# Kernel optimization log

Hardware: AMD Instinct MI355X
Metric: run time of the kernel (lower is better)

## Reference

```python
import jax, jax.numpy as jnp
import numpy as np

MAX_FRAMES = 4096  # static output capacity = T_phoneme * max_duration
PAD_VALUE = 0.0


def setup_inputs() -> dict:
    key = jax.random.key(0)
    k1, k2, k3, k4 = jax.random.split(key, 4)
    B, C, T = 16, 512, 512
    xs = jax.random.normal(k1, (B, C, T), dtype=jnp.float32)
    notepitch = jax.random.uniform(k2, (B, T), dtype=jnp.float32)
    ds = jax.random.randint(k3, (B, T), 0, 8, dtype=jnp.int32)
    x_lengths = jax.random.randint(k4, (B,), 0, 512, dtype=jnp.int32)
    return {"xs": xs, "notepitch": notepitch, "ds": ds, "x_lengths": x_lengths}


def _length_regulate(xs, notepitch, ds):
    # xs: (B, C, T), notepitch: (B, T), ds: (B, T) int durations
    # Replicate: ds[ds.sum(dim=1)==0] = 1 (fill all-zero duration rows with 1)
    row_zero = (ds.sum(axis=1) == 0)[:, None]  # (B, 1)
    ds = jnp.where(row_zero, jnp.ones_like(ds), ds)

    xs_t = jnp.transpose(xs, (0, 2, 1))  # (B, T, C)
    cum = jnp.cumsum(ds, axis=1)         # (B, T) exclusive-end offsets
    total = cum[:, -1]                   # (B,) frame lengths

    pos = jnp.arange(MAX_FRAMES, dtype=cum.dtype)  # (T_out,)
    # For each output frame position, which source token does it come from?
    # token j covers positions [cum[j-1], cum[j]) -> searchsorted(cum, pos, 'right')
    idx = jax.vmap(lambda c: jnp.searchsorted(c, pos, side="right"))(cum)  # (B, T_out)
    T = ds.shape[1]
    idx = jnp.clip(idx, 0, T - 1)
    mask = pos[None, :] < total[:, None]  # (B, T_out) valid frames

    # Gather expanded features: repeat_interleave as a gather
    out = jnp.take_along_axis(xs_t, idx[:, :, None], axis=1)  # (B, T_out, C)
    out = jnp.where(mask[:, :, None], out, jnp.asarray(PAD_VALUE, out.dtype))
    out = jnp.transpose(out, (0, 2, 1))  # (B, C, T_out)

    pitch = jnp.take_along_axis(notepitch, idx, axis=1)  # (B, T_out)
    pitch = jnp.where(mask, pitch, jnp.asarray(PAD_VALUE, pitch.dtype))
    return out, pitch, total


def reference(xs, notepitch, ds, x_lengths):
    # notepitch is detached in the original forward
    out, pitch, total = _length_regulate(xs, jax.lax.stop_gradient(notepitch), ds)
    return out, pitch, total.astype(jnp.int32)
```

## Files before the change

### kernel.cpp

```cpp
#include <hip/hip_runtime.h>

#define MAXF 4096

__global__ __launch_bounds__(512) void lr_prep(
    const float* __restrict__ notepitch,
    const int* __restrict__ ds,
    int* __restrict__ idx_ws,
    float* __restrict__ pitch_out,
    float* __restrict__ total_out,
    int T)
{
    const int b = blockIdx.x;
    const int t = threadIdx.x;

    __shared__ int cum[512];
    __shared__ int idx_sh[MAXF];

    int v = (t < T) ? ds[b * T + t] : 0;
    cum[t] = v;
    __syncthreads();

    for (int off = 1; off < 512; off <<= 1) {
        int x = cum[t];
        int y = (t >= off) ? cum[t - off] : 0;
        __syncthreads();
        cum[t] = x + y;
        __syncthreads();
    }

    int total = cum[T - 1];
    if (total == 0) {
        cum[t] = t + 1;
        total = T;
    }
    __syncthreads();

    for (int p = t; p < MAXF; p += 512) idx_sh[p] = -1;
    __syncthreads();

    if (t < T) {
        int lo = (t > 0) ? cum[t - 1] : 0;
        int hi = cum[t];
        for (int p = lo; p < hi; ++p) idx_sh[p] = t;
    }
    __syncthreads();

    for (int p = t; p < MAXF; p += 512) {
        int id = idx_sh[p];
        idx_ws[b * MAXF + p] = id;
        pitch_out[(size_t)b * MAXF + p] = (id >= 0) ? notepitch[b * T + id] : 0.0f;
    }
    if (t == 0) total_out[b] = (float)total;
}

__global__ __launch_bounds__(256) void lr_gather(
    const float* __restrict__ xs,
    const int* __restrict__ idx_ws,
    float* __restrict__ out,
    int T, int C)
{
    const int row = blockIdx.x;
    const int b = row / C;
    const float* __restrict__ xrow = xs + (size_t)row * T;
    const int* __restrict__ irow  = idx_ws + b * MAXF;
    float* __restrict__ orow      = out + (size_t)row * MAXF;

    const int t = threadIdx.x;
#pragma unroll
    for (int i = 0; i < MAXF / (256 * 4); ++i) {
        int p4 = (i * 256 + t) * 4;
        int4 id = *reinterpret_cast<const int4*>(irow + p4);
        float4 v;
        v.x = (id.x >= 0) ? xrow[id.x] : 0.0f;
        v.y = (id.y >= 0) ? xrow[id.y] : 0.0f;
        v.z = (id.z >= 0) ? xrow[id.z] : 0.0f;
        v.w = (id.w >= 0) ? xrow[id.w] : 0.0f;
        *reinterpret_cast<float4*>(orow + p4) = v;
    }
}

extern "C" void kernel_launch(void* const* d_in, const int* in_sizes, int n_in,
                              void* d_out, int out_size, void* d_ws, size_t ws_size,
                              hipStream_t stream) {
    const float* xs        = (const float*)d_in[0];
    const float* notepitch = (const float*)d_in[1];
    const int*   ds        = (const int*)d_in[2];

    const int B = in_sizes[3];
    const int T = in_sizes[1] / B;
    const int C = in_sizes[0] / (B * T);

    float* out       = (float*)d_out;
    float* pitch_out = out + (size_t)B * C * MAXF;
    float* total_out = pitch_out + (size_t)B * MAXF;

    int* idx_ws = (int*)d_ws;

    lr_prep<<<B, 512, 0, stream>>>(notepitch, ds, idx_ws, pitch_out, total_out, T);
    lr_gather<<<B * C, 256, 0, stream>>>(xs, idx_ws, out, T, C);
}
```

Baseline: 32.58 us.

## Fuse prefix-sum index build into gather kernel with channel grouping

Merges the prep and gather kernels into one. Each block recomputes the per-batch cumulative durations and frame index map in shared memory, then gathers 8 channels, so the global index workspace and the second launch go away. The scan is repeated C/8 times per batch, which adds redundant shared-memory work and barriers to every block. A clamp on the fill range to MAXF is also added.

```diff
diff --git a/kernel.cpp b/kernel.cpp
--- a/kernel.cpp
+++ b/kernel.cpp
@@ -1,17 +1,20 @@
 #include <hip/hip_runtime.h>
 
 #define MAXF 4096
+#define CG 8
 
-__global__ __launch_bounds__(512) void lr_prep(
+__global__ __launch_bounds__(512) void lr_fused(
+    const float* __restrict__ xs,
     const float* __restrict__ notepitch,
     const int* __restrict__ ds,
-    int* __restrict__ idx_ws,
+    float* __restrict__ out,
     float* __restrict__ pitch_out,
     float* __restrict__ total_out,
-    int T)
+    int T, int C)
 {
-    const int b = blockIdx.x;
-    const int t = threadIdx.x;
+    const int b  = blockIdx.y;
+    const int cg = blockIdx.x;
+    const int t  = threadIdx.x;
 
     __shared__ int cum[512];
     __shared__ int idx_sh[MAXF];
@@ -41,41 +44,36 @@
     if (t < T) {
         int lo = (t > 0) ? cum[t - 1] : 0;
         int hi = cum[t];
+        if (hi > MAXF) hi = MAXF;
         for (int p = lo; p < hi; ++p) idx_sh[p] = t;
     }
     __syncthreads();
 
-    for (int p = t; p < MAXF; p += 512) {
-        int id = idx_sh[p];
-        idx_ws[b * MAXF + p] = id;
-        pitch_out[(size_t)b * MAXF + p] = (id >= 0) ? notepitch[b * T + id] : 0.0f;
+    const float* __restrict__ xbase = xs  + ((size_t)b * C + (size_t)cg * CG) * T;
+    float* __restrict__       obase = out + ((size_t)b * C + (size_t)cg * CG) * MAXF;
+
+#pragma unroll
+    for (int i = 0; i < MAXF / (512 * 4); ++i) {
+        const int p4 = (i * 512 + t) * 4;
+        int4 id = *reinterpret_cast<const int4*>(&idx_sh[p4]);
+#pragma unroll
+        for (int ch = 0; ch < CG; ++ch) {
+            const float* __restrict__ xrow = xbase + (size_t)ch * T;
+            float4 vv;
+            vv.x = (id.x >= 0) ? xrow[id.x] : 0.0f;
+            vv.y = (id.y >= 0) ? xrow[id.y] : 0.0f;
+            vv.z = (id.z >= 0) ? xrow[id.z] : 0.0f;
+            vv.w = (id.w >= 0) ? xrow[id.w] : 0.0f;
+            *reinterpret_cast<float4*>(obase + (size_t)ch * MAXF + p4) = vv;
+        }
     }
-    if (t == 0) total_out[b] = (float)total;
-}
 
-__global__ __launch_bounds__(256) void lr_gather(
-    const float* __restrict__ xs,
-    const int* __restrict__ idx_ws,
-    float* __restrict__ out,
-    int T, int C)
-{
-    const int row = blockIdx.x;
-    const int b = row / C;
-    const float* __restrict__ xrow = xs + (size_t)row * T;
-    const int* __restrict__ irow  = idx_ws + b * MAXF;
-    float* __restrict__ orow      = out + (size_t)row * MAXF;
-
-    const int t = threadIdx.x;
-#pragma unroll
-    for (int i = 0; i < MAXF / (256 * 4); ++i) {
-        int p4 = (i * 256 + t) * 4;
-        int4 id = *reinterpret_cast<const int4*>(irow + p4);
-        float4 v;
-        v.x = (id.x >= 0) ? xrow[id.x] : 0.0f;
-        v.y = (id.y >= 0) ? xrow[id.y] : 0.0f;
-        v.z = (id.z >= 0) ? xrow[id.z] : 0.0f;
-        v.w = (id.w >= 0) ? xrow[id.w] : 0.0f;
-        *reinterpret_cast<float4*>(orow + p4) = v;
+    if (cg == 0) {
+        for (int p = t; p < MAXF; p += 512) {
+            int id = idx_sh[p];
+            pitch_out[(size_t)b * MAXF + p] = (id >= 0) ? notepitch[b * T + id] : 0.0f;
+        }
+        if (t == 0) total_out[b] = (float)total;
     }
 }
 
@@ -94,8 +92,6 @@
     float* pitch_out = out + (size_t)B * C * MAXF;
     float* total_out = pitch_out + (size_t)B * MAXF;
 
-    int* idx_ws = (int*)d_ws;
-
-    lr_prep<<<B, 512, 0, stream>>>(notepitch, ds, idx_ws, pitch_out, total_out, T);
-    lr_gather<<<B * C, 256, 0, stream>>>(xs, idx_ws, out, T, C);
+    dim3 grid(C / CG, B);
+    lr_fused<<<grid, 512, 0, stream>>>(xs, notepitch, ds, out, pitch_out, total_out, T, C);
 }
```

After: 28.75 us. 1.13x faster.
